# Kernel optimization log

Measured on AMD Instinct MI355X. Metric: run time of the kernel, lower is better.

The kernel has to match this reference:

```python
import jax, jax.numpy as jnp
import numpy as np


def setup_inputs() -> dict:
    key = jax.random.key(0)
    ks = jax.random.split(key, 6)
    B, C, S = 256, 2048, 7          # batch, embed_dim, spacial_dim
    OUT = 1024                      # output_dim
    return {
        "x": jax.random.normal(ks[0], (B, C, S, S), jnp.float32),
        "pos_emb": jax.random.normal(ks[1], (S * S + 1, C), jnp.float32) / (C ** 0.5),
        "Wv": jax.random.normal(ks[2], (C, C), jnp.float32) * 0.02,
        "bv": jnp.zeros((C,), jnp.float32),
        "Wc": jax.random.normal(ks[3], (OUT, C), jnp.float32) * 0.02,
        "bc": jnp.zeros((OUT,), jnp.float32),
        "num_heads": 32,
    }


def reference(x, pos_emb, Wv, bv, Wc, bc, num_heads):
    # x: [B, C, H, W] -> tokens [B, HW, C], prepend mean token -> [B, N, C]
    B, C, H, W = x.shape
    N = H * W + 1
    hd = C // num_heads
    scale = hd ** -0.5

    t = x.reshape(B, C, H * W).transpose(0, 2, 1)                    # [B, HW, C]
    t = jnp.concatenate([t.mean(axis=1, keepdims=True), t], axis=1)  # [B, N, C]
    t = t + pos_emb[None]                                            # add pos emb

    # qkv weights are all copies of v_proj => q = k = v = v_proj(t)
    v = t @ Wv.T + bv                                                # [B, N, C]
    vh = v.reshape(B, N, num_heads, hd).transpose(0, 2, 1, 3)        # [B, h, N, d]

    # attn_ori = softmax(q k^T * scale) with q=k=v; dropout p=0 (eval)
    attn = jax.nn.softmax(jnp.einsum('bhnd,bhmd->bhnm', vh, vh) * scale, axis=-1)
    ctx = jnp.einsum('bhnm,bhmd->bhnd', attn, vh)                    # [B, h, N, d]
    ctx = ctx.transpose(0, 2, 1, 3).reshape(B, N, C)

    # proj weights come from c_proj: [out_dim, C]
    x_ori = ctx @ Wc.T + bc                                          # [B, N, out]
    xout = v @ Wc.T + bc                                             # x-path: proj(v) directly
    # x[:, 0, :] = x_ori[:, 0, :]; module returns x (first list element)
    return xout.at[:, 0, :].set(x_ori[:, 0, :])
```

## Files before the change

kernel.cpp:

```cpp
#include <hip/hip_runtime.h>
#include <stdint.h>

#define BATCH  256
#define CDIM   2048
#define HW     49
#define NTOK   50
#define MROWS  (BATCH * NTOK)
#define ODIM   1024
#define NHEADS 32

typedef __attribute__((ext_vector_type(8))) short short8;
typedef __attribute__((ext_vector_type(4))) float f32x4;
typedef unsigned short u16;
typedef unsigned int   u32;

__device__ __forceinline__ float bf2f(u16 u) {
  union { u32 i; float f; } v; v.i = ((u32)u) << 16; return v.f;
}
__device__ __forceinline__ u16 f2bf(float f) {
  union { float f; u32 i; } v; v.f = f;
  u32 r = v.i + 0x7fffu + ((v.i >> 16) & 1u);
  return (u16)(r >> 16);
}

__device__ __forceinline__ void async16(const void* g, void* l) {
  __builtin_amdgcn_global_load_lds(
      (const __attribute__((address_space(1))) u32*)g,
      (__attribute__((address_space(3))) u32*)l, 16, 0, 0);
}

__global__ __launch_bounds__(256) void cvt2_kernel(const float* __restrict__ a,
                                                   u16* __restrict__ oa, int n4a,
                                                   const float* __restrict__ bsrc,
                                                   u16* __restrict__ ob, int n4b) {
  int i = blockIdx.x * 256 + threadIdx.x;
  const float* src; u16* dst; int idx;
  if (i < n4a) { src = a; dst = oa; idx = i; }
  else {
    idx = i - n4a;
    if (idx >= n4b) return;
    src = bsrc; dst = ob;
  }
  float4 v = reinterpret_cast<const float4*>(src)[idx];
  ushort4 o;
  o.x = f2bf(v.x); o.y = f2bf(v.y); o.z = f2bf(v.z); o.w = f2bf(v.w);
  reinterpret_cast<ushort4*>(dst)[idx] = o;
}

__global__ __launch_bounds__(256) void prep_kernel(const float* __restrict__ x,
                                                   const float* __restrict__ pos,
                                                   u16* __restrict__ T) {
  const int blk = blockIdx.x;
  const int b  = blk >> 5;
  const int c0 = (blk & 31) * 64;
  __shared__ float xs[64 * HW];
  __shared__ float mean[64];
  const float* src = x + ((size_t)b * CDIM + c0) * HW;
  for (int i = threadIdx.x; i < 64 * HW; i += 256) xs[i] = src[i];
  __syncthreads();
  if (threadIdx.x < 64) {
    float s = 0.f;
#pragma unroll
    for (int j = 0; j < HW; j++) s += xs[threadIdx.x * HW + j];
    mean[threadIdx.x] = s * (1.0f / 49.0f);
  }
  __syncthreads();
  for (int wi = threadIdx.x; wi < NTOK * 8; wi += 256) {
    const int n = wi >> 3;
    const int g = (wi & 7) * 8;
    alignas(16) u16 ov[8];
#pragma unroll
    for (int u = 0; u < 8; u++) {
      const int c = g + u;
      float val = (n == 0) ? mean[c] : xs[c * HW + (n - 1)];
      val += pos[n * CDIM + c0 + c];
      ov[u] = f2bf(val);
    }
    *reinterpret_cast<uint4*>(&T[((size_t)b * NTOK + n) * CDIM + c0 + g]) =
        *reinterpret_cast<const uint4*>(ov);
  }
}

template<int OUT_BF16>
__global__ __launch_bounds__(512, 2)
void gemm256(const u16* __restrict__ A, const u16* __restrict__ Bm,
             const float* __restrict__ bias, void* __restrict__ Cout,
             int M, int N, int K, int nbx) {
  __shared__ __align__(16) u16 smem[65536];

  const int NK = K >> 6;
  const int t = threadIdx.x;
  const int lane = t & 63;
  const int wid = t >> 6;
  const int wm = wid >> 2;
  const int wn = wid & 3;

  const int nwg = gridDim.x;
  const int cpx = nwg >> 3;
  const int orig = blockIdx.x;
  const int swz = (orig & 7) * cpx + (orig >> 3);
  const int bx = swz % nbx;
  const int by = swz / nbx;
  const int m0 = by * 256, n0 = bx * 256;

  const int tr  = t >> 3;
  const int to8 = ((t & 7) ^ (tr & 7)) << 3;
  const int t8  = t << 3;
  const u16* pA0 = A  + (size_t)(m0 + tr) * K + to8;
  const u16* pB0 = Bm + (size_t)(n0 + tr) * K + to8;

  const int lr = lane & 15, hi = lane >> 4;
  const int sx = lr & 7;
  const int aK0 = ((wm * 128 + lr) << 6) + (((0 + hi) ^ sx) << 3);
  const int aK1 = ((wm * 128 + lr) << 6) + (((4 + hi) ^ sx) << 3);
  const int bK0 = 16384 + ((wn * 64 + lr) << 6) + (((0 + hi) ^ sx) << 3);
  const int bK1 = 16384 + ((wn * 64 + lr) << 6) + (((4 + hi) ^ sx) << 3);

  f32x4 acc[8][4] = {};
  short8 a[4][2], b[2][2];

  auto STG = [&](int kti, int isB, int h) {
    if (kti < NK) {
      const u16* g = (isB ? pB0 : pA0) + (size_t)(h * 128) * K + kti * 64;
      u16* l = &smem[((kti & 1) << 15) + (isB << 14) + (h << 13) + t8];
      async16(g, l);
      async16(g + (size_t)64 * K, l + 4096);
    }
  };

  STG(0, 0, 0); STG(0, 0, 1); STG(0, 1, 0); STG(0, 1, 1); STG(1, 0, 0);
  asm volatile("s_waitcnt vmcnt(2)" ::: "memory");
  __builtin_amdgcn_s_barrier();

  for (int j = 0; j < NK; ++j) {
    const u16* sa = &smem[(j & 1) << 15];

#pragma unroll
    for (int f = 0; f < 4; ++f) {
      a[f][0] = *(const short8*)&sa[aK0 + f * 1024];
      a[f][1] = *(const short8*)&sa[aK1 + f * 1024];
    }
#pragma unroll
    for (int f = 0; f < 2; ++f) {
      b[f][0] = *(const short8*)&sa[bK0 + f * 1024];
      b[f][1] = *(const short8*)&sa[bK1 + f * 1024];
    }
    STG(j + 1, 0, 1);
    __builtin_amdgcn_s_barrier();
    asm volatile("s_waitcnt lgkmcnt(0)" ::: "memory");
    __builtin_amdgcn_sched_barrier(0);
    __builtin_amdgcn_s_setprio(1);
#pragma unroll
    for (int fm = 0; fm < 4; ++fm)
#pragma unroll
      for (int fn = 0; fn < 2; ++fn) {
        acc[fm][fn] = __builtin_amdgcn_mfma_f32_16x16x32_bf16(a[fm][0], b[fn][0], acc[fm][fn], 0, 0, 0);
        acc[fm][fn] = __builtin_amdgcn_mfma_f32_16x16x32_bf16(a[fm][1], b[fn][1], acc[fm][fn], 0, 0, 0);
      }
    __builtin_amdgcn_s_setprio(0);
    __builtin_amdgcn_s_barrier();

#pragma unroll
    for (int f = 0; f < 2; ++f) {
      b[f][0] = *(const short8*)&sa[bK0 + (2 + f) * 1024];
      b[f][1] = *(const short8*)&sa[bK1 + (2 + f) * 1024];
    }
    STG(j + 1, 1, 0);
    __builtin_amdgcn_s_barrier();
    asm volatile("s_waitcnt lgkmcnt(0)" ::: "memory");
    __builtin_amdgcn_sched_barrier(0);
    __builtin_amdgcn_s_setprio(1);
#pragma unroll
    for (int fm = 0; fm < 4; ++fm)
#pragma unroll
      for (int fn = 0; fn < 2; ++fn) {
        acc[fm][2 + fn] = __builtin_amdgcn_mfma_f32_16x16x32_bf16(a[fm][0], b[fn][0], acc[fm][2 + fn], 0, 0, 0);
        acc[fm][2 + fn] = __builtin_amdgcn_mfma_f32_16x16x32_bf16(a[fm][1], b[fn][1], acc[fm][2 + fn], 0, 0, 0);
      }
    __builtin_amdgcn_s_setprio(0);
    __builtin_amdgcn_s_barrier();

#pragma unroll
    for (int f = 0; f < 4; ++f) {
      a[f][0] = *(const short8*)&sa[aK0 + (4 + f) * 1024];
      a[f][1] = *(const short8*)&sa[aK1 + (4 + f) * 1024];
    }
    STG(j + 1, 1, 1);
    __builtin_amdgcn_s_barrier();
    asm volatile("s_waitcnt lgkmcnt(0)" ::: "memory");
    __builtin_amdgcn_sched_barrier(0);
    __builtin_amdgcn_s_setprio(1);
#pragma unroll
    for (int fm = 0; fm < 4; ++fm)
#pragma unroll
      for (int fn = 0; fn < 2; ++fn) {
        acc[4 + fm][2 + fn] = __builtin_amdgcn_mfma_f32_16x16x32_bf16(a[fm][0], b[fn][0], acc[4 + fm][2 + fn], 0, 0, 0);
        acc[4 + fm][2 + fn] = __builtin_amdgcn_mfma_f32_16x16x32_bf16(a[fm][1], b[fn][1], acc[4 + fm][2 + fn], 0, 0, 0);
      }
    __builtin_amdgcn_s_setprio(0);
    __builtin_amdgcn_s_barrier();

#pragma unroll
    for (int f = 0; f < 2; ++f) {
      b[f][0] = *(const short8*)&sa[bK0 + f * 1024];
      b[f][1] = *(const short8*)&sa[bK1 + f * 1024];
    }
    STG(j + 2, 0, 0);
    __builtin_amdgcn_s_barrier();
    asm volatile("s_waitcnt lgkmcnt(0)" ::: "memory");
    __builtin_amdgcn_sched_barrier(0);
    __builtin_amdgcn_s_setprio(1);
#pragma unroll
    for (int fm = 0; fm < 4; ++fm)
#pragma unroll
      for (int fn = 0; fn < 2; ++fn) {
        acc[4 + fm][fn] = __builtin_amdgcn_mfma_f32_16x16x32_bf16(a[fm][0], b[fn][0], acc[4 + fm][fn], 0, 0, 0);
        acc[4 + fm][fn] = __builtin_amdgcn_mfma_f32_16x16x32_bf16(a[fm][1], b[fn][1], acc[4 + fm][fn], 0, 0, 0);
      }
    __builtin_amdgcn_s_setprio(0);
    if (j < NK - 2) asm volatile("s_waitcnt vmcnt(2)" ::: "memory");
    else            asm volatile("s_waitcnt vmcnt(0)" ::: "memory");
    __builtin_amdgcn_s_barrier();
  }

  const int erow = hi * 4;
#pragma unroll
  for (int fm = 0; fm < 8; ++fm) {
#pragma unroll
    for (int fn = 0; fn < 4; ++fn) {
      const int cg = n0 + wn * 64 + fn * 16 + lr;
      const float bb = bias[cg];
      const int rbase = m0 + wm * 128 + fm * 16 + erow;
#pragma unroll
      for (int jr = 0; jr < 4; ++jr) {
        const float val = acc[fm][fn][jr] + bb;
        if (OUT_BF16)
          ((u16*)Cout)[(size_t)(rbase + jr) * N + cg] = f2bf(val);
        else
          ((float*)Cout)[(size_t)(rbase + jr) * N + cg] = val;
      }
    }
  }
}

__global__ __launch_bounds__(64) void attn0_kernel(u16* __restrict__ V) {
  const int b = blockIdx.x, h = blockIdx.y;
  __shared__ __align__(16) u16 vt[NTOK * 64];
  __shared__ float pb[64];
  const int t = threadIdx.x;
  u16* base = V + (size_t)b * NTOK * CDIM + h * 64;
  for (int idx = t; idx < NTOK * 8; idx += 64) {
    const int m = idx >> 3, g = (idx & 7) * 8;
    *reinterpret_cast<uint4*>(&vt[m * 64 + g]) =
        *reinterpret_cast<const uint4*>(base + (size_t)m * CDIM + g);
  }
  __syncthreads();
  const float qd = bf2f(vt[t]);
  float s_own = -1e30f;
  for (int m = 0; m < NTOK; m++) {
    float p = qd * bf2f(vt[m * 64 + t]);
#pragma unroll
    for (int off = 32; off; off >>= 1) p += __shfl_xor(p, off);
    if (t == m) s_own = p * 0.125f;
  }
  float mx = s_own;
#pragma unroll
  for (int off = 32; off; off >>= 1) mx = fmaxf(mx, __shfl_xor(mx, off));
  const float e = (t < NTOK) ? __expf(s_own - mx) : 0.f;
  float Z = e;
#pragma unroll
  for (int off = 32; off; off >>= 1) Z += __shfl_xor(Z, off);
  pb[t] = e / Z;
  __syncthreads();
  float acc = 0.f;
  for (int m = 0; m < NTOK; m++) acc += pb[m] * bf2f(vt[m * 64 + t]);
  base[t] = f2bf(acc);
}

extern "C" void kernel_launch(void* const* d_in, const int* in_sizes, int n_in,
                              void* d_out, int out_size, void* d_ws, size_t ws_size,
                              hipStream_t stream) {
  const float* x   = (const float*)d_in[0];
  const float* pos = (const float*)d_in[1];
  const float* Wv  = (const float*)d_in[2];
  const float* bv  = (const float*)d_in[3];
  const float* Wc  = (const float*)d_in[4];
  const float* bc  = (const float*)d_in[5];
  float* out = (float*)d_out;

  u16* T   = (u16*)d_ws;
  u16* V   = T   + (size_t)MROWS * CDIM;
  u16* WvB = V   + (size_t)MROWS * CDIM;
  u16* WcB = WvB + (size_t)CDIM * CDIM;

  {
    int n4a = CDIM * CDIM / 4;
    int n4b = ODIM * CDIM / 4;
    cvt2_kernel<<<(n4a + n4b + 255) / 256, 256, 0, stream>>>(Wv, WvB, n4a, Wc, WcB, n4b);
  }
  prep_kernel<<<BATCH * 32, 256, 0, stream>>>(x, pos, T);

  gemm256<1><<<(MROWS / 256) * (CDIM / 256), 512, 0, stream>>>(
      T, WvB, bv, V, MROWS, CDIM, CDIM, CDIM / 256);

  attn0_kernel<<<dim3(BATCH, NHEADS), 64, 0, stream>>>(V);

  gemm256<0><<<(MROWS / 256) * (ODIM / 256), 512, 0, stream>>>(
      V, WcB, bc, out, MROWS, ODIM, CDIM, ODIM / 256);
}
```

Measured before the change: 310.5 us.

## Software-pipeline LDS fragment loads with MFMA using ping-pong registers in GEMM

Restructures the GEMM main loop so LDS fragment reads for the next sub-tile are issued before the current MFMA batch, using double register sets (a0/a1, bA/bB) and partial lgkmcnt waits in place of full waits plus extra barriers. The loop is unrolled by two to alternate B register sets, and the next K-tile's first fragments are prefetched after the barrier. Also vectorizes the prep kernel's global-to-LDS copy with float4. This raises register pressure and relies on NK being even and on the lgkmcnt counts being exact.

```diff
diff --git a/kernel.cpp b/kernel.cpp
--- a/kernel.cpp
+++ b/kernel.cpp
@@ -56,7 +56,8 @@
   __shared__ float xs[64 * HW];
   __shared__ float mean[64];
   const float* src = x + ((size_t)b * CDIM + c0) * HW;
-  for (int i = threadIdx.x; i < 64 * HW; i += 256) xs[i] = src[i];
+  for (int i = threadIdx.x; i < 64 * HW / 4; i += 256)
+    reinterpret_cast<float4*>(xs)[i] = reinterpret_cast<const float4*>(src)[i];
   __syncthreads();
   if (threadIdx.x < 64) {
     float s = 0.f;
@@ -117,7 +118,7 @@
   const int bK1 = 16384 + ((wn * 64 + lr) << 6) + (((4 + hi) ^ sx) << 3);
 
   f32x4 acc[8][4] = {};
-  short8 a[4][2], b[2][2];
+  short8 a0[4][2], a1[4][2], bA[2][2], bB[2][2];
 
   auto STG = [&](int kti, int isB, int h) {
     if (kti < NK) {
@@ -128,99 +129,102 @@
     }
   };
 
+#define MFMA4x2(M0, N0, AARR, BARR)                                           \
+  _Pragma("unroll")                                                           \
+  for (int fm = 0; fm < 4; ++fm) {                                            \
+    _Pragma("unroll")                                                         \
+    for (int fn = 0; fn < 2; ++fn) {                                          \
+      acc[(M0) + fm][(N0) + fn] = __builtin_amdgcn_mfma_f32_16x16x32_bf16(    \
+          AARR[fm][0], BARR[fn][0], acc[(M0) + fm][(N0) + fn], 0, 0, 0);      \
+      acc[(M0) + fm][(N0) + fn] = __builtin_amdgcn_mfma_f32_16x16x32_bf16(    \
+          AARR[fm][1], BARR[fn][1], acc[(M0) + fm][(N0) + fn], 0, 0, 0);      \
+    }                                                                         \
+  }
+
+#define TILE(J, BLO, BHI)                                                     \
+  {                                                                           \
+    const u16* sa = &smem[((J) & 1) << 15];                                   \
+    const u16* sb = &smem[(((J) + 1) & 1) << 15];                             \
+                                                            \
+    STG((J) + 1, 0, 1);                                                       \
+    BHI[0][0] = *(const short8*)&sa[bK0 + 2048];                              \
+    BHI[0][1] = *(const short8*)&sa[bK1 + 2048];                              \
+    BHI[1][0] = *(const short8*)&sa[bK0 + 3072];                              \
+    BHI[1][1] = *(const short8*)&sa[bK1 + 3072];                              \
+    asm volatile("s_waitcnt lgkmcnt(4)" ::: "memory");                        \
+    __builtin_amdgcn_sched_barrier(0);                                        \
+    __builtin_amdgcn_s_setprio(1);                                            \
+    MFMA4x2(0, 0, a0, BLO);                                                   \
+    __builtin_amdgcn_s_setprio(0);                                            \
+    __builtin_amdgcn_s_barrier();                                             \
+                                                            \
+    STG((J) + 1, 1, 0);                                                       \
+    a1[0][0] = *(const short8*)&sa[aK0 + 4096];                               \
+    a1[0][1] = *(const short8*)&sa[aK1 + 4096];                               \
+    a1[1][0] = *(const short8*)&sa[aK0 + 5120];                               \
+    a1[1][1] = *(const short8*)&sa[aK1 + 5120];                               \
+    a1[2][0] = *(const short8*)&sa[aK0 + 6144];                               \
+    a1[2][1] = *(const short8*)&sa[aK1 + 6144];                               \
+    a1[3][0] = *(const short8*)&sa[aK0 + 7168];                               \
+    a1[3][1] = *(const short8*)&sa[aK1 + 7168];                               \
+    asm volatile("s_waitcnt lgkmcnt(8)" ::: "memory");                        \
+    __builtin_amdgcn_sched_barrier(0);                                        \
+    __builtin_amdgcn_s_setprio(1);                                            \
+    MFMA4x2(0, 2, a0, BHI);                                                   \
+    __builtin_amdgcn_s_setprio(0);                                            \
+                                                            \
+    STG((J) + 1, 1, 1);                                                       \
+    asm volatile("s_waitcnt lgkmcnt(0)" ::: "memory");                        \
+    __builtin_amdgcn_sched_barrier(0);                                        \
+    __builtin_amdgcn_s_setprio(1);                                            \
+    MFMA4x2(4, 2, a1, BHI);                                                   \
+    __builtin_amdgcn_s_setprio(0);                                            \
+                                                            \
+    STG((J) + 2, 0, 0);                                                       \
+    if ((J) < NK - 2) asm volatile("s_waitcnt vmcnt(2)" ::: "memory");        \
+    else              asm volatile("s_waitcnt vmcnt(0)" ::: "memory");        \
+    __builtin_amdgcn_s_barrier();                                             \
+    if ((J) + 1 < NK) {                                                       \
+      a0[0][0] = *(const short8*)&sb[aK0];                                    \
+      a0[0][1] = *(const short8*)&sb[aK1];                                    \
+      a0[1][0] = *(const short8*)&sb[aK0 + 1024];                             \
+      a0[1][1] = *(const short8*)&sb[aK1 + 1024];                             \
+      a0[2][0] = *(const short8*)&sb[aK0 + 2048];                             \
+      a0[2][1] = *(const short8*)&sb[aK1 + 2048];                             \
+      a0[3][0] = *(const short8*)&sb[aK0 + 3072];                             \
+      a0[3][1] = *(const short8*)&sb[aK1 + 3072];                             \
+      BHI[0][0] = *(const short8*)&sb[bK0];                                   \
+      BHI[0][1] = *(const short8*)&sb[bK1];                                   \
+      BHI[1][0] = *(const short8*)&sb[bK0 + 1024];                            \
+      BHI[1][1] = *(const short8*)&sb[bK1 + 1024];                            \
+    }                                                                         \
+    asm volatile("s_waitcnt lgkmcnt(12)" ::: "memory");                       \
+    __builtin_amdgcn_sched_barrier(0);                                        \
+    __builtin_amdgcn_s_setprio(1);                                            \
+    MFMA4x2(4, 0, a1, BLO);                                                   \
+    __builtin_amdgcn_s_setprio(0);                                            \
+  }
+
   STG(0, 0, 0); STG(0, 0, 1); STG(0, 1, 0); STG(0, 1, 1); STG(1, 0, 0);
   asm volatile("s_waitcnt vmcnt(2)" ::: "memory");
   __builtin_amdgcn_s_barrier();
 
-  for (int j = 0; j < NK; ++j) {
-    const u16* sa = &smem[(j & 1) << 15];
-
-#pragma unroll
-    for (int f = 0; f < 4; ++f) {
-      a[f][0] = *(const short8*)&sa[aK0 + f * 1024];
-      a[f][1] = *(const short8*)&sa[aK1 + f * 1024];
-    }
-#pragma unroll
-    for (int f = 0; f < 2; ++f) {
-      b[f][0] = *(const short8*)&sa[bK0 + f * 1024];
-      b[f][1] = *(const short8*)&sa[bK1 + f * 1024];
-    }
-    STG(j + 1, 0, 1);
-    __builtin_amdgcn_s_barrier();
-    asm volatile("s_waitcnt lgkmcnt(0)" ::: "memory");
-    __builtin_amdgcn_sched_barrier(0);
-    __builtin_amdgcn_s_setprio(1);
-#pragma unroll
-    for (int fm = 0; fm < 4; ++fm)
-#pragma unroll
-      for (int fn = 0; fn < 2; ++fn) {
-        acc[fm][fn] = __builtin_amdgcn_mfma_f32_16x16x32_bf16(a[fm][0], b[fn][0], acc[fm][fn], 0, 0, 0);
-        acc[fm][fn] = __builtin_amdgcn_mfma_f32_16x16x32_bf16(a[fm][1], b[fn][1], acc[fm][fn], 0, 0, 0);
-      }
-    __builtin_amdgcn_s_setprio(0);
-    __builtin_amdgcn_s_barrier();
-
-#pragma unroll
-    for (int f = 0; f < 2; ++f) {
-      b[f][0] = *(const short8*)&sa[bK0 + (2 + f) * 1024];
-      b[f][1] = *(const short8*)&sa[bK1 + (2 + f) * 1024];
-    }
-    STG(j + 1, 1, 0);
-    __builtin_amdgcn_s_barrier();
-    asm volatile("s_waitcnt lgkmcnt(0)" ::: "memory");
-    __builtin_amdgcn_sched_barrier(0);
-    __builtin_amdgcn_s_setprio(1);
-#pragma unroll
-    for (int fm = 0; fm < 4; ++fm)
-#pragma unroll
-      for (int fn = 0; fn < 2; ++fn) {
-        acc[fm][2 + fn] = __builtin_amdgcn_mfma_f32_16x16x32_bf16(a[fm][0], b[fn][0], acc[fm][2 + fn], 0, 0, 0);
-        acc[fm][2 + fn] = __builtin_amdgcn_mfma_f32_16x16x32_bf16(a[fm][1], b[fn][1], acc[fm][2 + fn], 0, 0, 0);
-      }
-    __builtin_amdgcn_s_setprio(0);
-    __builtin_amdgcn_s_barrier();
-
-#pragma unroll
-    for (int f = 0; f < 4; ++f) {
-      a[f][0] = *(const short8*)&sa[aK0 + (4 + f) * 1024];
-      a[f][1] = *(const short8*)&sa[aK1 + (4 + f) * 1024];
-    }
-    STG(j + 1, 1, 1);
-    __builtin_amdgcn_s_barrier();
-    asm volatile("s_waitcnt lgkmcnt(0)" ::: "memory");
-    __builtin_amdgcn_sched_barrier(0);
-    __builtin_amdgcn_s_setprio(1);
-#pragma unroll
-    for (int fm = 0; fm < 4; ++fm)
-#pragma unroll
-      for (int fn = 0; fn < 2; ++fn) {
-        acc[4 + fm][2 + fn] = __builtin_amdgcn_mfma_f32_16x16x32_bf16(a[fm][0], b[fn][0], acc[4 + fm][2 + fn], 0, 0, 0);
-        acc[4 + fm][2 + fn] = __builtin_amdgcn_mfma_f32_16x16x32_bf16(a[fm][1], b[fn][1], acc[4 + fm][2 + fn], 0, 0, 0);
-      }
-    __builtin_amdgcn_s_setprio(0);
-    __builtin_amdgcn_s_barrier();
-
-#pragma unroll
-    for (int f = 0; f < 2; ++f) {
-      b[f][0] = *(const short8*)&sa[bK0 + f * 1024];
-      b[f][1] = *(const short8*)&sa[bK1 + f * 1024];
-    }
-    STG(j + 2, 0, 0);
-    __builtin_amdgcn_s_barrier();
-    asm volatile("s_waitcnt lgkmcnt(0)" ::: "memory");
-    __builtin_amdgcn_sched_barrier(0);
-    __builtin_amdgcn_s_setprio(1);
-#pragma unroll
-    for (int fm = 0; fm < 4; ++fm)
-#pragma unroll
-      for (int fn = 0; fn < 2; ++fn) {
-        acc[4 + fm][fn] = __builtin_amdgcn_mfma_f32_16x16x32_bf16(a[fm][0], b[fn][0], acc[4 + fm][fn], 0, 0, 0);
-        acc[4 + fm][fn] = __builtin_amdgcn_mfma_f32_16x16x32_bf16(a[fm][1], b[fn][1], acc[4 + fm][fn], 0, 0, 0);
-      }
-    __builtin_amdgcn_s_setprio(0);
-    if (j < NK - 2) asm volatile("s_waitcnt vmcnt(2)" ::: "memory");
-    else            asm volatile("s_waitcnt vmcnt(0)" ::: "memory");
-    __builtin_amdgcn_s_barrier();
+  a0[0][0] = *(const short8*)&smem[aK0];
+  a0[0][1] = *(const short8*)&smem[aK1];
+  a0[1][0] = *(const short8*)&smem[aK0 + 1024];
+  a0[1][1] = *(const short8*)&smem[aK1 + 1024];
+  a0[2][0] = *(const short8*)&smem[aK0 + 2048];
+  a0[2][1] = *(const short8*)&smem[aK1 + 2048];
+  a0[3][0] = *(const short8*)&smem[aK0 + 3072];
+  a0[3][1] = *(const short8*)&smem[aK1 + 3072];
+  bA[0][0] = *(const short8*)&smem[bK0];
+  bA[0][1] = *(const short8*)&smem[bK1];
+  bA[1][0] = *(const short8*)&smem[bK0 + 1024];
+  bA[1][1] = *(const short8*)&smem[bK1 + 1024];
+
+  for (int j = 0; j < NK; j += 2) {
+    TILE(j,     bA, bB);
+    TILE(j + 1, bB, bA);
   }
 
   const int erow = hi * 4;
@@ -241,6 +245,8 @@
       }
     }
   }
+#undef TILE
+#undef MFMA4x2
 }
 
 __global__ __launch_bounds__(64) void attn0_kernel(u16* __restrict__ V) {
```

Measured after the change: 415.6 us. 1.34x slower.

## Switch GEMM to 32x32x16 MFMA tiles and fuse weight-convert with prep kernel

Applied to the files above, without the earlier changes.

Rewrites the GEMM inner loop to use 32x32x16 bf16 MFMA instructions with 16-wide accumulators instead of 16x16x32. The larger tiles cut the number of LDS fragment reads per FLOP and the MFMA instruction count. The epilogue is remapped to the 32x32 output layout. It also merges the weight-conversion and token-prep kernels into one launch, and vectorises the x load in prep to float4. The trade-off is different register pressure and LDS access patterns, plus row-scattered stores in the epilogue.

```diff
diff --git a/kernel.cpp b/kernel.cpp
--- a/kernel.cpp
+++ b/kernel.cpp
@@ -9,8 +9,9 @@
 #define ODIM   1024
 #define NHEADS 32
 
-typedef __attribute__((ext_vector_type(8))) short short8;
-typedef __attribute__((ext_vector_type(4))) float f32x4;
+typedef __attribute__((ext_vector_type(8)))  short short8;
+typedef __attribute__((ext_vector_type(4)))  float f32x4;
+typedef __attribute__((ext_vector_type(16))) float f32x16;
 typedef unsigned short u16;
 typedef unsigned int   u32;
 
@@ -29,34 +30,34 @@
       (__attribute__((address_space(3))) u32*)l, 16, 0, 0);
 }
 
-__global__ __launch_bounds__(256) void cvt2_kernel(const float* __restrict__ a,
-                                                   u16* __restrict__ oa, int n4a,
-                                                   const float* __restrict__ bsrc,
-                                                   u16* __restrict__ ob, int n4b) {
-  int i = blockIdx.x * 256 + threadIdx.x;
-  const float* src; u16* dst; int idx;
-  if (i < n4a) { src = a; dst = oa; idx = i; }
-  else {
-    idx = i - n4a;
-    if (idx >= n4b) return;
-    src = bsrc; dst = ob;
-  }
-  float4 v = reinterpret_cast<const float4*>(src)[idx];
-  ushort4 o;
-  o.x = f2bf(v.x); o.y = f2bf(v.y); o.z = f2bf(v.z); o.w = f2bf(v.w);
-  reinterpret_cast<ushort4*>(dst)[idx] = o;
-}
-
-__global__ __launch_bounds__(256) void prep_kernel(const float* __restrict__ x,
-                                                   const float* __restrict__ pos,
-                                                   u16* __restrict__ T) {
-  const int blk = blockIdx.x;
+__global__ __launch_bounds__(256) void cvt_prep_kernel(
+    const float* __restrict__ Wv, u16* __restrict__ WvB, int n4a,
+    const float* __restrict__ Wc, u16* __restrict__ WcB, int n4b,
+    const float* __restrict__ x, const float* __restrict__ pos,
+    u16* __restrict__ T, int nCvt) {
+  if (blockIdx.x < (unsigned)nCvt) {
+    int i = blockIdx.x * 256 + threadIdx.x;
+    const float* src; u16* dst; int idx;
+    if (i < n4a) { src = Wv; dst = WvB; idx = i; }
+    else {
+      idx = i - n4a;
+      if (idx >= n4b) return;
+      src = Wc; dst = WcB;
+    }
+    float4 v = reinterpret_cast<const float4*>(src)[idx];
+    ushort4 o;
+    o.x = f2bf(v.x); o.y = f2bf(v.y); o.z = f2bf(v.z); o.w = f2bf(v.w);
+    reinterpret_cast<ushort4*>(dst)[idx] = o;
+    return;
+  }
+  const int blk = blockIdx.x - nCvt;
   const int b  = blk >> 5;
   const int c0 = (blk & 31) * 64;
   __shared__ float xs[64 * HW];
   __shared__ float mean[64];
   const float* src = x + ((size_t)b * CDIM + c0) * HW;
-  for (int i = threadIdx.x; i < 64 * HW; i += 256) xs[i] = src[i];
+  for (int i = threadIdx.x; i < 64 * HW / 4; i += 256)
+    reinterpret_cast<float4*>(xs)[i] = reinterpret_cast<const float4*>(src)[i];
   __syncthreads();
   if (threadIdx.x < 64) {
     float s = 0.f;
@@ -109,15 +110,16 @@
   const u16* pA0 = A  + (size_t)(m0 + tr) * K + to8;
   const u16* pB0 = Bm + (size_t)(n0 + tr) * K + to8;
 
-  const int lr = lane & 15, hi = lane >> 4;
-  const int sx = lr & 7;
-  const int aK0 = ((wm * 128 + lr) << 6) + (((0 + hi) ^ sx) << 3);
-  const int aK1 = ((wm * 128 + lr) << 6) + (((4 + hi) ^ sx) << 3);
-  const int bK0 = 16384 + ((wn * 64 + lr) << 6) + (((0 + hi) ^ sx) << 3);
-  const int bK1 = 16384 + ((wn * 64 + lr) << 6) + (((4 + hi) ^ sx) << 3);
-
-  f32x4 acc[8][4] = {};
-  short8 a[4][2], b[2][2];
+  const int l31 = lane & 31, hi5 = lane >> 5;
+  const int sx = l31 & 7;
+  int aG[4];
+#pragma unroll
+  for (int kq = 0; kq < 4; ++kq) aG[kq] = (((kq * 2 + hi5) ^ sx) << 3);
+  const int aBase = ((wm * 128 + l31) << 6);
+  const int bBase = 16384 + ((wn * 64 + l31) << 6);
+
+  f32x16 acc[4][2] = {};
+  short8 a[2][4], a2[2][4], b[4];
 
   auto STG = [&](int kti, int isB, int h) {
     if (kti < NK) {
@@ -128,6 +130,15 @@
     }
   };
 
+#define MFMAQ(MT0, NT, AARR)                                                  \
+  _Pragma("unroll")                                                           \
+  for (int kq = 0; kq < 4; ++kq) {                                            \
+    acc[(MT0)][(NT)] = __builtin_amdgcn_mfma_f32_32x32x16_bf16(               \
+        AARR[0][kq], b[kq], acc[(MT0)][(NT)], 0, 0, 0);                       \
+    acc[(MT0) + 1][(NT)] = __builtin_amdgcn_mfma_f32_32x32x16_bf16(           \
+        AARR[1][kq], b[kq], acc[(MT0) + 1][(NT)], 0, 0, 0);                   \
+  }
+
   STG(0, 0, 0); STG(0, 0, 1); STG(0, 1, 0); STG(0, 1, 1); STG(1, 0, 0);
   asm volatile("s_waitcnt vmcnt(2)" ::: "memory");
   __builtin_amdgcn_s_barrier();
@@ -136,111 +147,82 @@
     const u16* sa = &smem[(j & 1) << 15];
 
 #pragma unroll
-    for (int f = 0; f < 4; ++f) {
-      a[f][0] = *(const short8*)&sa[aK0 + f * 1024];
-      a[f][1] = *(const short8*)&sa[aK1 + f * 1024];
-    }
-#pragma unroll
-    for (int f = 0; f < 2; ++f) {
-      b[f][0] = *(const short8*)&sa[bK0 + f * 1024];
-      b[f][1] = *(const short8*)&sa[bK1 + f * 1024];
-    }
+    for (int mt = 0; mt < 2; ++mt)
+#pragma unroll
+      for (int kq = 0; kq < 4; ++kq)
+        a[mt][kq] = *(const short8*)&sa[aBase + mt * 2048 + aG[kq]];
+#pragma unroll
+    for (int kq = 0; kq < 4; ++kq)
+      b[kq] = *(const short8*)&sa[bBase + aG[kq]];
     STG(j + 1, 0, 1);
     __builtin_amdgcn_s_barrier();
     asm volatile("s_waitcnt lgkmcnt(0)" ::: "memory");
     __builtin_amdgcn_sched_barrier(0);
     __builtin_amdgcn_s_setprio(1);
-#pragma unroll
-    for (int fm = 0; fm < 4; ++fm)
-#pragma unroll
-      for (int fn = 0; fn < 2; ++fn) {
-        acc[fm][fn] = __builtin_amdgcn_mfma_f32_16x16x32_bf16(a[fm][0], b[fn][0], acc[fm][fn], 0, 0, 0);
-        acc[fm][fn] = __builtin_amdgcn_mfma_f32_16x16x32_bf16(a[fm][1], b[fn][1], acc[fm][fn], 0, 0, 0);
-      }
-    __builtin_amdgcn_s_setprio(0);
-    __builtin_amdgcn_s_barrier();
-
-#pragma unroll
-    for (int f = 0; f < 2; ++f) {
-      b[f][0] = *(const short8*)&sa[bK0 + (2 + f) * 1024];
-      b[f][1] = *(const short8*)&sa[bK1 + (2 + f) * 1024];
-    }
+    MFMAQ(0, 0, a);
+    __builtin_amdgcn_s_setprio(0);
+    __builtin_amdgcn_s_barrier();
+
+#pragma unroll
+    for (int kq = 0; kq < 4; ++kq)
+      b[kq] = *(const short8*)&sa[bBase + 2048 + aG[kq]];
     STG(j + 1, 1, 0);
     __builtin_amdgcn_s_barrier();
     asm volatile("s_waitcnt lgkmcnt(0)" ::: "memory");
     __builtin_amdgcn_sched_barrier(0);
     __builtin_amdgcn_s_setprio(1);
-#pragma unroll
-    for (int fm = 0; fm < 4; ++fm)
-#pragma unroll
-      for (int fn = 0; fn < 2; ++fn) {
-        acc[fm][2 + fn] = __builtin_amdgcn_mfma_f32_16x16x32_bf16(a[fm][0], b[fn][0], acc[fm][2 + fn], 0, 0, 0);
-        acc[fm][2 + fn] = __builtin_amdgcn_mfma_f32_16x16x32_bf16(a[fm][1], b[fn][1], acc[fm][2 + fn], 0, 0, 0);
-      }
-    __builtin_amdgcn_s_setprio(0);
-    __builtin_amdgcn_s_barrier();
-
-#pragma unroll
-    for (int f = 0; f < 4; ++f) {
-      a[f][0] = *(const short8*)&sa[aK0 + (4 + f) * 1024];
-      a[f][1] = *(const short8*)&sa[aK1 + (4 + f) * 1024];
-    }
+    MFMAQ(0, 1, a);
+    __builtin_amdgcn_s_setprio(0);
+    __builtin_amdgcn_s_barrier();
+
+#pragma unroll
+    for (int mt = 0; mt < 2; ++mt)
+#pragma unroll
+      for (int kq = 0; kq < 4; ++kq)
+        a2[mt][kq] = *(const short8*)&sa[aBase + (2 + mt) * 2048 + aG[kq]];
     STG(j + 1, 1, 1);
     __builtin_amdgcn_s_barrier();
     asm volatile("s_waitcnt lgkmcnt(0)" ::: "memory");
     __builtin_amdgcn_sched_barrier(0);
     __builtin_amdgcn_s_setprio(1);
-#pragma unroll
-    for (int fm = 0; fm < 4; ++fm)
-#pragma unroll
-      for (int fn = 0; fn < 2; ++fn) {
-        acc[4 + fm][2 + fn] = __builtin_amdgcn_mfma_f32_16x16x32_bf16(a[fm][0], b[fn][0], acc[4 + fm][2 + fn], 0, 0, 0);
-        acc[4 + fm][2 + fn] = __builtin_amdgcn_mfma_f32_16x16x32_bf16(a[fm][1], b[fn][1], acc[4 + fm][2 + fn], 0, 0, 0);
-      }
-    __builtin_amdgcn_s_setprio(0);
-    __builtin_amdgcn_s_barrier();
-
-#pragma unroll
-    for (int f = 0; f < 2; ++f) {
-      b[f][0] = *(const short8*)&sa[bK0 + f * 1024];
-      b[f][1] = *(const short8*)&sa[bK1 + f * 1024];
-    }
+    MFMAQ(2, 1, a2);
+    __builtin_amdgcn_s_setprio(0);
+    __builtin_amdgcn_s_barrier();
+
+#pragma unroll
+    for (int kq = 0; kq < 4; ++kq)
+      b[kq] = *(const short8*)&sa[bBase + aG[kq]];
     STG(j + 2, 0, 0);
     __builtin_amdgcn_s_barrier();
     asm volatile("s_waitcnt lgkmcnt(0)" ::: "memory");
     __builtin_amdgcn_sched_barrier(0);
     __builtin_amdgcn_s_setprio(1);
-#pragma unroll
-    for (int fm = 0; fm < 4; ++fm)
-#pragma unroll
-      for (int fn = 0; fn < 2; ++fn) {
-        acc[4 + fm][fn] = __builtin_amdgcn_mfma_f32_16x16x32_bf16(a[fm][0], b[fn][0], acc[4 + fm][fn], 0, 0, 0);
-        acc[4 + fm][fn] = __builtin_amdgcn_mfma_f32_16x16x32_bf16(a[fm][1], b[fn][1], acc[4 + fm][fn], 0, 0, 0);
-      }
+    MFMAQ(2, 0, a2);
     __builtin_amdgcn_s_setprio(0);
     if (j < NK - 2) asm volatile("s_waitcnt vmcnt(2)" ::: "memory");
     else            asm volatile("s_waitcnt vmcnt(0)" ::: "memory");
     __builtin_amdgcn_s_barrier();
   }
 
-  const int erow = hi * 4;
-#pragma unroll
-  for (int fm = 0; fm < 8; ++fm) {
-#pragma unroll
-    for (int fn = 0; fn < 4; ++fn) {
-      const int cg = n0 + wn * 64 + fn * 16 + lr;
+#pragma unroll
+  for (int mt = 0; mt < 4; ++mt) {
+#pragma unroll
+    for (int nt = 0; nt < 2; ++nt) {
+      const int cg = n0 + wn * 64 + nt * 32 + l31;
       const float bb = bias[cg];
-      const int rbase = m0 + wm * 128 + fm * 16 + erow;
-#pragma unroll
-      for (int jr = 0; jr < 4; ++jr) {
-        const float val = acc[fm][fn][jr] + bb;
+      const int rb = m0 + wm * 128 + mt * 32 + 4 * hi5;
+#pragma unroll
+      for (int r = 0; r < 16; ++r) {
+        const int rg = rb + (r & 3) + 8 * (r >> 2);
+        const float val = acc[mt][nt][r] + bb;
         if (OUT_BF16)
-          ((u16*)Cout)[(size_t)(rbase + jr) * N + cg] = f2bf(val);
+          ((u16*)Cout)[(size_t)rg * N + cg] = f2bf(val);
         else
-          ((float*)Cout)[(size_t)(rbase + jr) * N + cg] = val;
+          ((float*)Cout)[(size_t)rg * N + cg] = val;
       }
     }
   }
+#undef MFMAQ
 }
 
 __global__ __launch_bounds__(64) void attn0_kernel(u16* __restrict__ V) {
@@ -296,9 +278,10 @@
   {
     int n4a = CDIM * CDIM / 4;
     int n4b = ODIM * CDIM / 4;
-    cvt2_kernel<<<(n4a + n4b + 255) / 256, 256, 0, stream>>>(Wv, WvB, n4a, Wc, WcB, n4b);
-  }
-  prep_kernel<<<BATCH * 32, 256, 0, stream>>>(x, pos, T);
+    int nCvt = (n4a + n4b + 255) / 256;
+    cvt_prep_kernel<<<nCvt + BATCH * 32, 256, 0, stream>>>(
+        Wv, WvB, n4a, Wc, WcB, n4b, x, pos, T, nCvt);
+  }
 
   gemm256<1><<<(MROWS / 256) * (CDIM / 256), 512, 0, stream>>>(
       T, WvB, bv, V, MROWS, CDIM, CDIM, CDIM / 256);
```

Result: faster. 292.1 us (-5.9%).
